# Performance work log

Hardware: AMD Instinct MI355X
Metric: run time of the kernel (lower is better)

## Reference

```python
import jax, jax.numpy as jnp
import numpy as np

THRESHOLD = 0.5
MAX_POINTS = 10000
NORMALIZE = True
BIDIRECTIONAL = True
INF = jnp.float32(1e30)


def _voxels_to_points(vox):
    # vox: (D, H, W). Returns padded points (MAX_POINTS, 3) and validity mask.
    D, H, W = vox.shape
    flat = vox.reshape(-1)
    active = flat > THRESHOLD
    n_active = jnp.sum(active.astype(jnp.int32))
    # Stable argsort puts active voxel indices first (deterministic stand-in
    # for torch's randperm subsampling when n_active > MAX_POINTS).
    order = jnp.argsort(jnp.where(active, 0, 1).astype(jnp.int32))
    idx = order[:MAX_POINTS]
    valid = jnp.arange(MAX_POINTS) < jnp.minimum(n_active, MAX_POINTS)
    d = idx // (H * W)
    h = (idx // W) % H
    w = idx % W
    pts = jnp.stack([d, h, w], axis=-1).astype(jnp.float32)  # (MAX_POINTS, 3)
    if NORMALIZE:
        pts = pts / (D - 1) * 2.0 - 1.0
    pts = jnp.where(valid[:, None], pts, 0.0)
    return pts, valid


def _chamfer_single(p1, v1, p2, v2):
    # p1: (N,3), p2: (M,3) padded; v1/v2 are validity masks.
    n1 = jnp.sum(p1 * p1, axis=1)  # (N,)
    n2 = jnp.sum(p2 * p2, axis=1)  # (M,)
    dist = n1[:, None] + n2[None, :] - 2.0 * (p1 @ p2.T)  # (N, M)
    dist = jnp.maximum(dist, 0.0)
    c1 = jnp.maximum(jnp.sum(v1.astype(jnp.float32)), 1.0)
    c2 = jnp.maximum(jnp.sum(v2.astype(jnp.float32)), 1.0)
    min_1to2 = jnp.min(jnp.where(v2[None, :], dist, INF), axis=1)  # (N,)
    loss = jnp.sum(jnp.where(v1, min_1to2, 0.0)) / c1
    if BIDIRECTIONAL:
        min_2to1 = jnp.min(jnp.where(v1[:, None], dist, INF), axis=0)  # (M,)
        loss = loss + jnp.sum(jnp.where(v2, min_2to1, 0.0)) / c2
    return loss


def setup_inputs() -> dict:
    key = jax.random.key(0)
    k1, k2 = jax.random.split(key)
    pred = jax.random.uniform(k1, (4, 1, 64, 64, 64), dtype=jnp.float32)
    target = jax.random.uniform(k2, (4, 1, 64, 64, 64), dtype=jnp.float32)
    return {"pred": pred, "target": target}


def reference(pred, target):
    B = pred.shape[0]
    total = jnp.float32(0.0)
    n_valid = jnp.float32(0.0)
    for b in range(B):  # small fixed batch loop (per-sample dist matrix is 10k x 10k)
        p1, v1 = _voxels_to_points(pred[b, 0])
        p2, v2 = _voxels_to_points(target[b, 0])
        has_pts = jnp.logical_and(jnp.any(v1), jnp.any(v2))
        cd = _chamfer_single(p1, v1, p2, v2)
        total = total + jnp.where(has_pts, cd, 0.0)
        n_valid = n_valid + has_pts.astype(jnp.float32)
    return jnp.where(n_valid > 0, total / jnp.maximum(n_valid, 1.0), 0.0)
```

## Files before the change

### kernel.cpp

```cpp
#include <hip/hip_runtime.h>
#include <hip/hip_bf16.h>


#define NVOX      262144
#define NCHUNK    256
#define MAXPTS    10000
#define PTS_PAD   10240
#define NCLOUD    8
#define NTASK     8
#define NRB       40
#define QPB       512
#define NQB       20
#define RSPLIT    8
#define RLEN      1280
#define CH_REFS   640
#define CH_STEPS  10
#define NCH       2
#define SCALE     (2.0f/63.0f)

typedef _Float16 half8  __attribute__((ext_vector_type(8)));
typedef float    f32x16 __attribute__((ext_vector_type(16)));

#define WS_TOTALS   0
#define WS_COUNTS   1024
#define WS_OFFSETS  16384
#define WS_QFRAG    32768
#define WS_RFRAG    1343488
#define WS_NQ       2654208
#define WS_SMIN     2981888
#define WS_BSUM     5603328

__device__ __forceinline__ const float* cloud_src(const float* pred, const float* tgt, int cloud) {
    const float* base = (cloud & 1) ? tgt : pred;
    return base + (size_t)(cloud >> 1) * NVOX;
}

__global__ void k_count(const float* __restrict__ pred, const float* __restrict__ tgt,
                        int* __restrict__ counts,
                        half8* __restrict__ Qfrag, half8* __restrict__ Rfrag,
                        float* __restrict__ nqint) {
    int gi = blockIdx.x * 256 + threadIdx.x;
    if (gi < NCLOUD * PTS_PAD) {
        half8 zq = {0, 0, 0, 0, 0, 0, 0, 0};
        half8 zr = {0, 0, 0, (_Float16)4096, 0, 0, 0, 0};
        Qfrag[gi] = zq;
        Rfrag[gi] = zr;
        nqint[gi] = 0.f;
    }
    int cloud = blockIdx.x >> 8;
    int chunk = blockIdx.x & 255;
    int t = threadIdx.x;
    const float* src = cloud_src(pred, tgt, cloud) + chunk * 1024;
    float4 v = reinterpret_cast<const float4*>(src)[t];
    int cnt = (v.x > 0.5f) + (v.y > 0.5f) + (v.z > 0.5f) + (v.w > 0.5f);
    __shared__ int s[256];
    s[t] = cnt; __syncthreads();
    for (int o = 128; o > 0; o >>= 1) {
        if (t < o) s[t] += s[t + o];
        __syncthreads();
    }
    if (t == 0) counts[cloud * NCHUNK + chunk] = s[0];
}

__global__ void k_scan(const int* __restrict__ counts, int* __restrict__ offsets,
                       int* __restrict__ totals) {
    int cloud = blockIdx.x;
    int t = threadIdx.x;
    int c = counts[cloud * NCHUNK + t];
    __shared__ int s[256];
    s[t] = c; __syncthreads();
    for (int o = 1; o < 256; o <<= 1) {
        int v = (t >= o) ? s[t - o] : 0;
        __syncthreads();
        s[t] += v;
        __syncthreads();
    }
    offsets[cloud * NCHUNK + t] = s[t] - c;
    if (t == 255) totals[cloud] = s[255];
}

__global__ void k_compact(const float* __restrict__ pred, const float* __restrict__ tgt,
                          const int* __restrict__ offsets,
                          half8* __restrict__ Qfrag, half8* __restrict__ Rfrag,
                          float* __restrict__ nqint) {
    int cloud = blockIdx.x >> 8;
    int chunk = blockIdx.x & 255;
    int t = threadIdx.x;
    const float* src = cloud_src(pred, tgt, cloud) + chunk * 1024;
    float4 v = reinterpret_cast<const float4*>(src)[t];
    int f0 = v.x > 0.5f, f1 = v.y > 0.5f, f2 = v.z > 0.5f, f3 = v.w > 0.5f;
    int cnt = f0 + f1 + f2 + f3;
    __shared__ int s[256];
    s[t] = cnt; __syncthreads();
    for (int o = 1; o < 256; o <<= 1) {
        int x = (t >= o) ? s[t - o] : 0;
        __syncthreads();
        s[t] += x;
        __syncthreads();
    }
    int rank = offsets[cloud * NCHUNK + chunk] + (s[t] - cnt);
    int eidx = chunk * 1024 + t * 4;
    int flags[4] = {f0, f1, f2, f3};
    size_t base = (size_t)cloud * PTS_PAD;
    #pragma unroll
    for (int e = 0; e < 4; ++e) {
        if (flags[e]) {
            if (rank < MAXPTS) {
                int idx = eidx + e;
                int d = idx >> 12, h = (idx >> 6) & 63, w = idx & 63;
                int nr = d * d + h * h + w * w;
                half8 Q = {(_Float16)(-2 * d), (_Float16)(-2 * h), (_Float16)(-2 * w),
                           (_Float16)8, (_Float16)1, 0, 0, 0};
                half8 R = {(_Float16)d, (_Float16)h, (_Float16)w,
                           (_Float16)(nr >> 3), (_Float16)(nr & 7), 0, 0, 0};
                Qfrag[base + rank] = Q;
                Rfrag[base + rank] = R;
                nqint[base + rank] = (float)nr;
            }
            rank++;
        }
    }
}

__device__ __forceinline__ float red16(f32x16 d, float m) {
    float t0 = fminf(fminf(d[0], d[1]), d[2]);
    float t1 = fminf(fminf(d[3], d[4]), d[5]);
    float t2 = fminf(fminf(d[6], d[7]), d[8]);
    float t3 = fminf(fminf(d[9], d[10]), d[11]);
    float t4 = fminf(fminf(d[12], d[13]), d[14]);
    float t5 = fminf(d[15], m);
    float u0 = fminf(fminf(t0, t1), t2);
    float u1 = fminf(fminf(t3, t4), t5);
    return fminf(u0, u1);
}

#define MFMA_MIN(aa, bb, mm)                                                      \
    do {                                                                          \
        f32x16 d_ = __builtin_amdgcn_mfma_f32_32x32x16_f16((aa), (bb), cz, 0, 0, 0); \
        asm("" : "+v"(d_));                                                       \
        (mm) = red16(d_, (mm));                                                   \
    } while (0)

__global__ __launch_bounds__(256, 4) void k_chamfer(const half8* __restrict__ Qfrag,
                                                    const half8* __restrict__ Rfrag,
                                                    float* __restrict__ smin) {
    int task = blockIdx.x / (NQB * RSPLIT);
    int rem  = blockIdx.x % (NQB * RSPLIT);
    int qb   = rem / RSPLIT;
    int rs   = rem % RSPLIT;
    int b = task >> 1, dir = task & 1;
    int qc = 2 * b + dir;
    int rc = 2 * b + (dir ^ 1);
    int tid = threadIdx.x, wave = tid >> 6, lane = tid & 63;

    __shared__ float4 ldsv[CH_REFS];
    char* lds = (char*)ldsv;

    int qbase = qb * QPB + wave * 128;
    half8 zero8 = {0, 0, 0, 0, 0, 0, 0, 0};
    half8 bq0 = zero8, bq1 = zero8, bq2 = zero8, bq3 = zero8;
    if (lane < 32) {
        const half8* qp = Qfrag + (size_t)qc * PTS_PAD + qbase + lane;
        bq0 = qp[0]; bq1 = qp[32]; bq2 = qp[64]; bq3 = qp[96];
    }
    float m0 = 1e30f, m1 = 1e30f, m2 = 1e30f, m3 = 1e30f;
    f32x16 cz;
    #pragma unroll
    for (int e = 0; e < 16; ++e) cz[e] = 0.f;

    const float4* Rsrc = (const float4*)(Rfrag + (size_t)rc * PTS_PAD + rs * RLEN);
    const char* rdbase = lds + (lane & 31) * 16;

    for (int c = 0; c < NCH; ++c) {
        __syncthreads();
        const float4* src = Rsrc + c * CH_REFS;
        for (int i = tid; i < CH_REFS; i += 256) ldsv[i] = src[i];
        __syncthreads();
        #pragma unroll 2
        for (int t = 0; t < CH_STEPS; ++t) {
            half8 a0 = *(const half8*)(rdbase + t * 1024);
            half8 a1 = *(const half8*)(rdbase + t * 1024 + 512);
            MFMA_MIN(a0, bq0, m0);
            MFMA_MIN(a1, bq0, m0);
            MFMA_MIN(a0, bq1, m1);
            MFMA_MIN(a1, bq1, m1);
            MFMA_MIN(a0, bq2, m2);
            MFMA_MIN(a1, bq2, m2);
            MFMA_MIN(a0, bq3, m3);
            MFMA_MIN(a1, bq3, m3);
        }
    }

    m0 = fminf(m0, __shfl_xor(m0, 32));
    m1 = fminf(m1, __shfl_xor(m1, 32));
    m2 = fminf(m2, __shfl_xor(m2, 32));
    m3 = fminf(m3, __shfl_xor(m3, 32));
    if (lane < 32) {
        float* outp = smin + ((size_t)task * RSPLIT + rs) * PTS_PAD + qbase + lane;
        outp[0]  = m0;
        outp[32] = m1;
        outp[64] = m2;
        outp[96] = m3;
    }
}

__global__ void k_reduce(const float* __restrict__ nqint, const int* __restrict__ totals,
                         const float* __restrict__ smin, float* __restrict__ bsum) {
    int task = blockIdx.x / NRB;
    int rb   = blockIdx.x % NRB;
    int tid  = threadIdx.x;
    int qi   = rb * 256 + tid;
    int qc   = 2 * (task >> 1) + (task & 1);
    int countQ = min(totals[qc], MAXPTS);

    const float SC2 = SCALE * SCALE;
    float contrib = 0.f;
    if (qi < countQ) {
        const float* s = smin + (size_t)task * RSPLIT * PTS_PAD + qi;
        float m = fminf(fminf(s[0 * PTS_PAD], s[1 * PTS_PAD]),
                        fminf(s[2 * PTS_PAD], s[3 * PTS_PAD]));
        m = fminf(m, fminf(fminf(s[4 * PTS_PAD], s[5 * PTS_PAD]),
                           fminf(s[6 * PTS_PAD], s[7 * PTS_PAD])));
        float nq = nqint[(size_t)qc * PTS_PAD + qi];
        contrib = fmaxf((nq + m) * SC2, 0.f);
    }
    __shared__ float sb[256];
    sb[tid] = contrib; __syncthreads();
    for (int o = 128; o > 0; o >>= 1) {
        if (tid < o) sb[tid] += sb[tid + o];
        __syncthreads();
    }
    if (tid == 0) bsum[task * NRB + rb] = sb[0];
}

__global__ void k_final(const float* __restrict__ bsum, const int* __restrict__ totals,
                        float* __restrict__ out) {
    float total = 0.f, nv = 0.f;
    for (int b = 0; b < 4; ++b) {
        float s1 = 0.f, s2 = 0.f;
        for (int i = 0; i < NRB; ++i) {
            s1 += bsum[(2 * b) * NRB + i];
            s2 += bsum[(2 * b + 1) * NRB + i];
        }
        int c1 = min(totals[2 * b], MAXPTS);
        int c2 = min(totals[2 * b + 1], MAXPTS);
        float cd = s1 / fmaxf((float)c1, 1.f) + s2 / fmaxf((float)c2, 1.f);
        if (c1 > 0 && c2 > 0) { total += cd; nv += 1.f; }
    }
    out[0] = (nv > 0.f) ? total / nv : 0.f;
}

extern "C" void kernel_launch(void* const* d_in, const int* in_sizes, int n_in,
                              void* d_out, int out_size, void* d_ws, size_t ws_size,
                              hipStream_t stream) {
    const float* pred = (const float*)d_in[0];
    const float* tgt  = (const float*)d_in[1];
    float* out = (float*)d_out;

    char* ws = (char*)d_ws;
    int*   totals  = (int*)(ws + WS_TOTALS);
    int*   counts  = (int*)(ws + WS_COUNTS);
    int*   offsets = (int*)(ws + WS_OFFSETS);
    half8* Qfrag   = (half8*)(ws + WS_QFRAG);
    half8* Rfrag   = (half8*)(ws + WS_RFRAG);
    float* nqint   = (float*)(ws + WS_NQ);
    float* smin    = (float*)(ws + WS_SMIN);
    float* bsum    = (float*)(ws + WS_BSUM);

    k_count  <<<NCLOUD * NCHUNK, 256, 0, stream>>>(pred, tgt, counts, Qfrag, Rfrag, nqint);
    k_scan   <<<NCLOUD,          256, 0, stream>>>(counts, offsets, totals);
    k_compact<<<NCLOUD * NCHUNK, 256, 0, stream>>>(pred, tgt, offsets, Qfrag, Rfrag, nqint);
    k_chamfer<<<NTASK * NQB * RSPLIT, 256, 0, stream>>>(Qfrag, Rfrag, smin);
    k_reduce <<<NTASK * NRB,     256, 0, stream>>>(nqint, totals, smin, bsum);
    k_final  <<<1, 1, 0, stream>>>(bsum, totals, out);
}
```

Before: 48.34 us.

## Switch chamfer MFMA to 16x16x32 tiles and drop LDS staging of references

Replaces the 32x32x16 MFMA with 16x16x32 f16 MFMA, keeping eight query fragments per wave in registers. Reference fragments now come straight from global memory, read by lanes 0-15, while the other lanes point at a zero padding region. This removes the shared-memory staging and the two block barriers per chunk. Each MFMA now yields 4 outputs instead of 16, so the min-reduction work per MFMA shrinks. The trade-off is more MFMA issues per unit of work, and reference loads that are no longer shared through LDS across waves.

```diff
diff --git a/kernel.cpp b/kernel.cpp
--- a/kernel.cpp
+++ b/kernel.cpp
@@ -9,17 +9,16 @@
 #define NCLOUD    8
 #define NTASK     8
 #define NRB       40
+#define QPW       128
 #define QPB       512
 #define NQB       20
 #define RSPLIT    8
 #define RLEN      1280
-#define CH_REFS   640
-#define CH_STEPS  10
-#define NCH       2
+#define RSTEPS    80
 #define SCALE     (2.0f/63.0f)
 
-typedef _Float16 half8  __attribute__((ext_vector_type(8)));
-typedef float    f32x16 __attribute__((ext_vector_type(16)));
+typedef _Float16 half8 __attribute__((ext_vector_type(8)));
+typedef float    f32x4 __attribute__((ext_vector_type(4)));
 
 #define WS_TOTALS   0
 #define WS_COUNTS   1024
@@ -122,25 +121,6 @@
     }
 }
 
-__device__ __forceinline__ float red16(f32x16 d, float m) {
-    float t0 = fminf(fminf(d[0], d[1]), d[2]);
-    float t1 = fminf(fminf(d[3], d[4]), d[5]);
-    float t2 = fminf(fminf(d[6], d[7]), d[8]);
-    float t3 = fminf(fminf(d[9], d[10]), d[11]);
-    float t4 = fminf(fminf(d[12], d[13]), d[14]);
-    float t5 = fminf(d[15], m);
-    float u0 = fminf(fminf(t0, t1), t2);
-    float u1 = fminf(fminf(t3, t4), t5);
-    return fminf(u0, u1);
-}
-
-#define MFMA_MIN(aa, bb, mm)                                                      \
-    do {                                                                          \
-        f32x16 d_ = __builtin_amdgcn_mfma_f32_32x32x16_f16((aa), (bb), cz, 0, 0, 0); \
-        asm("" : "+v"(d_));                                                       \
-        (mm) = red16(d_, (mm));                                                   \
-    } while (0)
-
 __global__ __launch_bounds__(256, 4) void k_chamfer(const half8* __restrict__ Qfrag,
                                                     const half8* __restrict__ Rfrag,
                                                     float* __restrict__ smin) {
@@ -152,55 +132,51 @@
     int qc = 2 * b + dir;
     int rc = 2 * b + (dir ^ 1);
     int tid = threadIdx.x, wave = tid >> 6, lane = tid & 63;
-
-    __shared__ float4 ldsv[CH_REFS];
-    char* lds = (char*)ldsv;
-
-    int qbase = qb * QPB + wave * 128;
-    half8 zero8 = {0, 0, 0, 0, 0, 0, 0, 0};
-    half8 bq0 = zero8, bq1 = zero8, bq2 = zero8, bq3 = zero8;
-    if (lane < 32) {
-        const half8* qp = Qfrag + (size_t)qc * PTS_PAD + qbase + lane;
-        bq0 = qp[0]; bq1 = qp[32]; bq2 = qp[64]; bq3 = qp[96];
-    }
-    float m0 = 1e30f, m1 = 1e30f, m2 = 1e30f, m3 = 1e30f;
-    f32x16 cz;
-    #pragma unroll
-    for (int e = 0; e < 16; ++e) cz[e] = 0.f;
-
-    const float4* Rsrc = (const float4*)(Rfrag + (size_t)rc * PTS_PAD + rs * RLEN);
-    const char* rdbase = lds + (lane & 31) * 16;
-
-    for (int c = 0; c < NCH; ++c) {
-        __syncthreads();
-        const float4* src = Rsrc + c * CH_REFS;
-        for (int i = tid; i < CH_REFS; i += 256) ldsv[i] = src[i];
-        __syncthreads();
-        #pragma unroll 2
-        for (int t = 0; t < CH_STEPS; ++t) {
-            half8 a0 = *(const half8*)(rdbase + t * 1024);
-            half8 a1 = *(const half8*)(rdbase + t * 1024 + 512);
-            MFMA_MIN(a0, bq0, m0);
-            MFMA_MIN(a1, bq0, m0);
-            MFMA_MIN(a0, bq1, m1);
-            MFMA_MIN(a1, bq1, m1);
-            MFMA_MIN(a0, bq2, m2);
-            MFMA_MIN(a1, bq2, m2);
-            MFMA_MIN(a0, bq3, m3);
-            MFMA_MIN(a1, bq3, m3);
+    int l16 = lane & 15;
+
+    int qbase = qb * QPB + wave * QPW;
+    const half8* qp = Qfrag + (size_t)qc * PTS_PAD + qbase + l16;
+    half8 bq[8];
+    #pragma unroll
+    for (int f = 0; f < 8; ++f) bq[f] = qp[f * 16];
+
+    float m[8];
+    #pragma unroll
+    for (int f = 0; f < 8; ++f) m[f] = 1e30f;
+    f32x4 cz4 = {0.f, 0.f, 0.f, 0.f};
+
+    const char* rbase;
+    int rstep;
+    if (lane < 16) {
+        rbase = (const char*)(Rfrag + (size_t)rc * PTS_PAD + rs * RLEN + l16);
+        rstep = 16 * 16;
+    } else {
+        rbase = (const char*)(Qfrag + MAXPTS + 100);
+        rstep = 0;
+    }
+
+    #pragma unroll 4
+    for (int t = 0; t < RSTEPS; ++t) {
+        half8 a = *(const half8*)rbase;
+        rbase += rstep;
+        #pragma unroll
+        for (int f = 0; f < 8; ++f) {
+            f32x4 d_ = __builtin_amdgcn_mfma_f32_16x16x32_f16(a, bq[f], cz4, 0, 0, 0);
+            asm("" : "+v"(d_));
+            float t_ = fminf(fminf(d_[0], d_[1]), d_[2]);
+            m[f] = fminf(fminf(m[f], t_), d_[3]);
         }
     }
 
-    m0 = fminf(m0, __shfl_xor(m0, 32));
-    m1 = fminf(m1, __shfl_xor(m1, 32));
-    m2 = fminf(m2, __shfl_xor(m2, 32));
-    m3 = fminf(m3, __shfl_xor(m3, 32));
-    if (lane < 32) {
-        float* outp = smin + ((size_t)task * RSPLIT + rs) * PTS_PAD + qbase + lane;
-        outp[0]  = m0;
-        outp[32] = m1;
-        outp[64] = m2;
-        outp[96] = m3;
+    #pragma unroll
+    for (int f = 0; f < 8; ++f) {
+        m[f] = fminf(m[f], __shfl_xor(m[f], 16));
+        m[f] = fminf(m[f], __shfl_xor(m[f], 32));
+    }
+    if (lane < 16) {
+        float* outp = smin + ((size_t)task * RSPLIT + rs) * PTS_PAD + qbase + l16;
+        #pragma unroll
+        for (int f = 0; f < 8; ++f) outp[f * 16] = m[f];
     }
 }
 
@@ -217,12 +193,12 @@
     float contrib = 0.f;
     if (qi < countQ) {
         const float* s = smin + (size_t)task * RSPLIT * PTS_PAD + qi;
-        float m = fminf(fminf(s[0 * PTS_PAD], s[1 * PTS_PAD]),
-                        fminf(s[2 * PTS_PAD], s[3 * PTS_PAD]));
-        m = fminf(m, fminf(fminf(s[4 * PTS_PAD], s[5 * PTS_PAD]),
-                           fminf(s[6 * PTS_PAD], s[7 * PTS_PAD])));
+        float mn = fminf(fminf(s[0 * PTS_PAD], s[1 * PTS_PAD]),
+                         fminf(s[2 * PTS_PAD], s[3 * PTS_PAD]));
+        mn = fminf(mn, fminf(fminf(s[4 * PTS_PAD], s[5 * PTS_PAD]),
+                             fminf(s[6 * PTS_PAD], s[7 * PTS_PAD])));
         float nq = nqint[(size_t)qc * PTS_PAD + qi];
-        contrib = fmaxf((nq + m) * SC2, 0.f);
+        contrib = fmaxf((nq + mn) * SC2, 0.f);
     }
     __shared__ float sb[256];
     sb[tid] = contrib; __syncthreads();
```

New measurement: 63.28 us. 1.31x slower.

## Stream reference fragments from global with prefetch, widen per-wave query tile

Applied to the files above, without the earlier changes.

The chamfer kernel no longer stages reference fragments through LDS with block-wide barriers. Each wave now loads its reference fragment straight from global memory and prefetches the next step while the current one computes. Per-wave queries grow from 128 to 160 (five B fragments), so each A fragment is reused across more MFMAs, and the grid shrinks from 20 to 16 query blocks. The MFMAs are issued in inline asm batches followed by fixed s_nop padding. That padding guarantees result availability but may waste issue slots, and every wave now reads the same reference data independently from global or L2.

```diff
diff --git a/kernel.cpp b/kernel.cpp
--- a/kernel.cpp
+++ b/kernel.cpp
@@ -9,13 +9,12 @@
 #define NCLOUD    8
 #define NTASK     8
 #define NRB       40
-#define QPB       512
-#define NQB       20
+#define QPW       160
+#define QPB       640
+#define NQB       16
 #define RSPLIT    8
 #define RLEN      1280
-#define CH_REFS   640
-#define CH_STEPS  10
-#define NCH       2
+#define RSTEPS    40
 #define SCALE     (2.0f/63.0f)
 
 typedef _Float16 half8  __attribute__((ext_vector_type(8)));
@@ -134,73 +133,77 @@
     return fminf(u0, u1);
 }
 
-#define MFMA_MIN(aa, bb, mm)                                                      \
-    do {                                                                          \
-        f32x16 d_ = __builtin_amdgcn_mfma_f32_32x32x16_f16((aa), (bb), cz, 0, 0, 0); \
-        asm("" : "+v"(d_));                                                       \
-        (mm) = red16(d_, (mm));                                                   \
-    } while (0)
-
 __global__ __launch_bounds__(256, 4) void k_chamfer(const half8* __restrict__ Qfrag,
                                                     const half8* __restrict__ Rfrag,
                                                     float* __restrict__ smin) {
-    int task = blockIdx.x / (NQB * RSPLIT);
-    int rem  = blockIdx.x % (NQB * RSPLIT);
-    int qb   = rem / RSPLIT;
-    int rs   = rem % RSPLIT;
+    int task = blockIdx.x >> 7;
+    int rem  = blockIdx.x & 127;
+    int qb   = rem >> 3;
+    int rs   = rem & 7;
     int b = task >> 1, dir = task & 1;
     int qc = 2 * b + dir;
     int rc = 2 * b + (dir ^ 1);
     int tid = threadIdx.x, wave = tid >> 6, lane = tid & 63;
-
-    __shared__ float4 ldsv[CH_REFS];
-    char* lds = (char*)ldsv;
-
-    int qbase = qb * QPB + wave * 128;
+    int l32 = lane & 31;
+
+    int qbase = qb * QPB + wave * QPW;
     half8 zero8 = {0, 0, 0, 0, 0, 0, 0, 0};
-    half8 bq0 = zero8, bq1 = zero8, bq2 = zero8, bq3 = zero8;
+    half8 bq0 = zero8, bq1 = zero8, bq2 = zero8, bq3 = zero8, bq4 = zero8;
     if (lane < 32) {
-        const half8* qp = Qfrag + (size_t)qc * PTS_PAD + qbase + lane;
-        bq0 = qp[0]; bq1 = qp[32]; bq2 = qp[64]; bq3 = qp[96];
-    }
-    float m0 = 1e30f, m1 = 1e30f, m2 = 1e30f, m3 = 1e30f;
+        const half8* qp = Qfrag + (size_t)qc * PTS_PAD + qbase + l32;
+        bq0 = qp[0]; bq1 = qp[32]; bq2 = qp[64]; bq3 = qp[96]; bq4 = qp[128];
+    }
+    float m0 = 1e30f, m1 = 1e30f, m2 = 1e30f, m3 = 1e30f, m4 = 1e30f;
     f32x16 cz;
     #pragma unroll
     for (int e = 0; e < 16; ++e) cz[e] = 0.f;
 
-    const float4* Rsrc = (const float4*)(Rfrag + (size_t)rc * PTS_PAD + rs * RLEN);
-    const char* rdbase = lds + (lane & 31) * 16;
-
-    for (int c = 0; c < NCH; ++c) {
-        __syncthreads();
-        const float4* src = Rsrc + c * CH_REFS;
-        for (int i = tid; i < CH_REFS; i += 256) ldsv[i] = src[i];
-        __syncthreads();
-        #pragma unroll 2
-        for (int t = 0; t < CH_STEPS; ++t) {
-            half8 a0 = *(const half8*)(rdbase + t * 1024);
-            half8 a1 = *(const half8*)(rdbase + t * 1024 + 512);
-            MFMA_MIN(a0, bq0, m0);
-            MFMA_MIN(a1, bq0, m0);
-            MFMA_MIN(a0, bq1, m1);
-            MFMA_MIN(a1, bq1, m1);
-            MFMA_MIN(a0, bq2, m2);
-            MFMA_MIN(a1, bq2, m2);
-            MFMA_MIN(a0, bq3, m3);
-            MFMA_MIN(a1, bq3, m3);
-        }
-    }
+    const half8* rp = Rfrag + (size_t)rc * PTS_PAD + rs * RLEN + l32;
+    half8 a = *rp;
+
+#define STEP(aa)                                                               \
+    do {                                                                       \
+        f32x16 d0_, d1_, d2_;                                                  \
+        asm("v_mfma_f32_32x32x16_f16 %0, %3, %4, %7\n\t"                       \
+            "v_mfma_f32_32x32x16_f16 %1, %3, %5, %7\n\t"                       \
+            "v_mfma_f32_32x32x16_f16 %2, %3, %6, %7\n\t"                       \
+            "s_nop 7\n\ts_nop 7\n\ts_nop 7"                                    \
+            : "=v"(d0_), "=v"(d1_), "=v"(d2_)                                  \
+            : "v"(aa), "v"(bq0), "v"(bq1), "v"(bq2), "v"(cz));                 \
+        m0 = red16(d0_, m0);                                                   \
+        m1 = red16(d1_, m1);                                                   \
+        m2 = red16(d2_, m2);                                                   \
+        f32x16 e0_, e1_;                                                       \
+        asm("v_mfma_f32_32x32x16_f16 %0, %2, %3, %5\n\t"                       \
+            "v_mfma_f32_32x32x16_f16 %1, %2, %4, %5\n\t"                       \
+            "s_nop 7\n\ts_nop 7\n\ts_nop 7"                                    \
+            : "=v"(e0_), "=v"(e1_)                                             \
+            : "v"(aa), "v"(bq3), "v"(bq4), "v"(cz));                           \
+        m3 = red16(e0_, m3);                                                   \
+        m4 = red16(e1_, m4);                                                   \
+    } while (0)
+
+    for (int t = 0; t < RSTEPS - 1; ++t) {
+        rp += 32;
+        half8 an = *rp;
+        STEP(a);
+        a = an;
+    }
+    STEP(a);
+#undef STEP
 
     m0 = fminf(m0, __shfl_xor(m0, 32));
     m1 = fminf(m1, __shfl_xor(m1, 32));
     m2 = fminf(m2, __shfl_xor(m2, 32));
     m3 = fminf(m3, __shfl_xor(m3, 32));
+    m4 = fminf(m4, __shfl_xor(m4, 32));
     if (lane < 32) {
-        float* outp = smin + ((size_t)task * RSPLIT + rs) * PTS_PAD + qbase + lane;
-        outp[0]  = m0;
-        outp[32] = m1;
-        outp[64] = m2;
-        outp[96] = m3;
+        float* outp = smin + ((size_t)task * RSPLIT + rs) * PTS_PAD + qbase + l32;
+        outp[0]   = m0;
+        outp[32]  = m1;
+        outp[64]  = m2;
+        outp[96]  = m3;
+        outp[128] = m4;
     }
 }
 
@@ -217,12 +220,12 @@
     float contrib = 0.f;
     if (qi < countQ) {
         const float* s = smin + (size_t)task * RSPLIT * PTS_PAD + qi;
-        float m = fminf(fminf(s[0 * PTS_PAD], s[1 * PTS_PAD]),
-                        fminf(s[2 * PTS_PAD], s[3 * PTS_PAD]));
-        m = fminf(m, fminf(fminf(s[4 * PTS_PAD], s[5 * PTS_PAD]),
-                           fminf(s[6 * PTS_PAD], s[7 * PTS_PAD])));
+        float mn = fminf(fminf(s[0 * PTS_PAD], s[1 * PTS_PAD]),
+                         fminf(s[2 * PTS_PAD], s[3 * PTS_PAD]));
+        mn = fminf(mn, fminf(fminf(s[4 * PTS_PAD], s[5 * PTS_PAD]),
+                             fminf(s[6 * PTS_PAD], s[7 * PTS_PAD])));
         float nq = nqint[(size_t)qc * PTS_PAD + qi];
-        contrib = fmaxf((nq + m) * SC2, 0.f);
+        contrib = fmaxf((nq + mn) * SC2, 0.f);
     }
     __shared__ float sb[256];
     sb[tid] = contrib; __syncthreads();
```

Result: slower. 60.59 us (+25.3%).
